# Kernel tuning notes

Measured on AMD Instinct MI355X. Metric: run time of the kernel, lower is better.

## Reference

```python
import math
import jax, jax.numpy as jnp
import numpy as np

N_HEADS = 16
D_EMBED = 1024
D_HEAD = D_EMBED // N_HEADS
BATCH = 2
SEQ = 2048


def setup_inputs() -> dict:
    key = jax.random.key(0)
    k1, k2, k3 = jax.random.split(key, 3)
    scale = 1.0 / math.sqrt(D_EMBED)
    return {
        "x": jax.random.normal(k1, (1, BATCH, SEQ, D_EMBED), dtype=jnp.float32),
        "w_in": jax.random.normal(k2, (3 * D_EMBED, D_EMBED), dtype=jnp.float32) * scale,
        "b_in": jnp.zeros((3 * D_EMBED,), dtype=jnp.float32),
        "w_out": jax.random.normal(k3, (D_EMBED, D_EMBED), dtype=jnp.float32) * scale,
        "b_out": jnp.zeros((D_EMBED,), dtype=jnp.float32),
        "causal_mask": 1,
    }


def reference(x, w_in, b_in, w_out, b_out, causal_mask):
    lead, B, S, D = x.shape  # lead == 1
    H, dh = N_HEADS, D_HEAD
    # fused QKV projection (torch Linear: x @ W^T + b)
    qkv = jnp.einsum("lbsd,ed->lbse", x, w_in) + b_in
    q, k, v = jnp.split(qkv, 3, axis=-1)
    # [1,B,S,D] -> [B,H,S,dh]
    def to_heads(t):
        return t.reshape(B, S, H, dh).transpose(0, 2, 1, 3)
    q, k, v = to_heads(q), to_heads(k), to_heads(v)
    # scaled dot-product attention with optional causal mask
    scores = jnp.einsum("bhqd,bhkd->bhqk", q, k)
    if causal_mask:
        mask = jnp.triu(jnp.ones((S, S), dtype=bool), k=1)
        scores = jnp.where(mask, -jnp.inf, scores)
    scores = scores / math.sqrt(dh)
    attn = jax.nn.softmax(scores, axis=-1)
    out = jnp.einsum("bhqk,bhkd->bhqd", attn, v)
    out = out.transpose(0, 2, 1, 3).reshape(lead, B, S, D)
    return jnp.einsum("lbsd,ed->lbse", out, w_out) + b_out
```

## Files before the change

kernel.cpp:

```cpp
#include <hip/hip_runtime.h>
#include <hip/hip_bf16.h>
#include <stdint.h>

#define S_LEN 2048
#define D_EMB 1024
#define NHEAD 16
#define DHEAD 64
#define NBATCH 2
#define MROWS 4096

typedef __attribute__((ext_vector_type(8))) short bf16x8;
typedef __attribute__((ext_vector_type(4))) float f32x4;
typedef unsigned short u16;
typedef unsigned int u32;

__device__ __forceinline__ u16 f2bf(float f) {
  union { float f; u32 u; } v; v.f = f;
  u32 r = v.u + 0x7fffu + ((v.u >> 16) & 1u);
  return (u16)(r >> 16);
}

__device__ __forceinline__ void gl_lds16(const void* g, void* l) {
  __builtin_amdgcn_global_load_lds(
      (const __attribute__((address_space(1))) u32*)g,
      (__attribute__((address_space(3))) u32*)l, 16, 0, 0);
}

__device__ __forceinline__ int swz(int o) { return o ^ (((o >> 7) & 7) << 4); }

__global__ void cast_f32_bf16(const float* __restrict__ in, u16* __restrict__ out, int n4) {
  int i = blockIdx.x * blockDim.x + threadIdx.x;
  if (i < n4) {
    float4 v = reinterpret_cast<const float4*>(in)[i];
    ushort4 o;
    o.x = f2bf(v.x); o.y = f2bf(v.y); o.z = f2bf(v.z); o.w = f2bf(v.w);
    reinterpret_cast<ushort4*>(out)[i] = o;
  }
}

template <int EPI>
__launch_bounds__(512, 2)
__global__ void gemm_pipe(const u16* __restrict__ A, const u16* __restrict__ Bm,
                          const float* __restrict__ bias, int N,
                          u16* __restrict__ q_out, u16* __restrict__ k_out,
                          u16* __restrict__ vt_out, float* __restrict__ f_out) {
  __shared__ __align__(16) u16 As[4][128 * 64];
  __shared__ __align__(16) u16 Bs[4][128 * 64];
  const int K = 1024, NT = 16;
  const int t = threadIdx.x, w = t >> 6, lane = t & 63;
  const int lr = lane & 15, lg = lane >> 4;
  const int m0 = blockIdx.y * 128, n0 = blockIdx.x * 128;
  const int wr = w >> 2, wc = w & 3;

  f32x4 acc[4][2] = {};

  const int srow = w * 8 + (lane >> 3);
  const int scol = ((lane & 7) ^ (lane >> 3)) * 8;
  const u16* Asrc = A + (size_t)(m0 + srow) * K + scol;
  const u16* Bsrc = Bm + (size_t)(n0 + srow) * K + scol;

#define STAGEP(T)                                                        \
  do {                                                                   \
    const int _kt = (T) * 64, _bf = (T) & 3;                             \
    gl_lds16(Asrc + _kt, &As[_bf][w * 512]);                             \
    gl_lds16(Asrc + (size_t)64 * K + _kt, &As[_bf][4096 + w * 512]);     \
    gl_lds16(Bsrc + _kt, &Bs[_bf][w * 512]);                             \
    gl_lds16(Bsrc + (size_t)64 * K + _kt, &Bs[_bf][4096 + w * 512]);     \
  } while (0)

  const int xorv = (lane & 7) << 4;
  const int ofk[2] = {(lg * 16) ^ xorv, (64 + lg * 16) ^ xorv};

  STAGEP(0);
  STAGEP(1);
  STAGEP(2);

  for (int kt = 0; kt < NT; kt++) {
    if (kt < NT - 2)      asm volatile("s_waitcnt vmcnt(8)" ::: "memory");
    else if (kt == NT - 2) asm volatile("s_waitcnt vmcnt(4)" ::: "memory");
    else                   asm volatile("s_waitcnt vmcnt(0)" ::: "memory");
    __builtin_amdgcn_s_barrier();

    if (kt + 3 < NT) STAGEP(kt + 3);

    const char* Ab = (const char*)&As[kt & 3][0];
    const char* Bb = (const char*)&Bs[kt & 3][0];
#pragma unroll
    for (int ks = 0; ks < 2; ks++) {
      bf16x8 bfr[2];
#pragma unroll
      for (int j = 0; j < 2; j++)
        bfr[j] = *(const bf16x8*)(Bb + (wc * 32 + j * 16 + lr) * 128 + ofk[ks]);
#pragma unroll
      for (int i = 0; i < 4; i++) {
        bf16x8 af = *(const bf16x8*)(Ab + (wr * 64 + i * 16 + lr) * 128 + ofk[ks]);
#pragma unroll
        for (int j = 0; j < 2; j++)
          acc[i][j] = __builtin_amdgcn_mfma_f32_16x16x32_bf16(af, bfr[j], acc[i][j], 0, 0, 0);
      }
    }
  }
#undef STAGEP

#pragma unroll
  for (int j = 0; j < 2; j++) {
    const int n = n0 + wc * 32 + j * 16 + lr;
    const float bv = bias[n];
    const int which = n >> 10, nn = n & 1023;
    const int h = nn >> 6, d = nn & 63;
#pragma unroll
    for (int i = 0; i < 4; i++) {
#pragma unroll
      for (int r = 0; r < 4; r++) {
        const int m = m0 + wr * 64 + i * 16 + lg * 4 + r;
        float v = acc[i][j][r] + bv;
        if (EPI == 0) {
          const int b = m >> 11, s = m & 2047;
          if (which == 0)
            q_out[(size_t)(((b * NHEAD + h) * S_LEN) + s) * DHEAD + d] = f2bf(v * 0.180336880f);
          else if (which == 1)
            k_out[(size_t)(((b * NHEAD + h) * S_LEN) + s) * DHEAD + d] = f2bf(v);
          else
            vt_out[(size_t)(((b * NHEAD + h) * DHEAD) + d) * S_LEN + s] = f2bf(v);
        } else {
          f_out[(size_t)m * N + n] = v;
        }
      }
    }
  }
}

__launch_bounds__(512, 2)
__global__ void attn_kernel(const u16* __restrict__ Qg, const u16* __restrict__ Kg,
                            const u16* __restrict__ Vtg, u16* __restrict__ AO,
                            const int* __restrict__ causal) {
  __shared__ __align__(16) u16 Kt[2][64 * 64];
  __shared__ __align__(16) u16 Vt[2][64 * 64];
  __shared__ __align__(16) u16 Pl[8][16 * 72];

  const int t = threadIdx.x, w = t >> 6, lane = t & 63;
  const int lr = lane & 15, lg = lane >> 4;
  const int nqt = (int)gridDim.x;
  const int qt = ((int)blockIdx.y < 16) ? (nqt - 1 - (int)blockIdx.x) : (int)blockIdx.x;
  const int bh = blockIdx.y;
  const size_t bh_off = (size_t)bh * S_LEN * DHEAD;
  const int cz = *causal;
  const int q0 = qt * 128;
  const int nk = cz ? (2 * qt + 2) : (S_LEN / 64);

  bf16x8 ones;
#pragma unroll
  for (int e = 0; e < 8; e++) ones[e] = (short)16256;

  {
    const char* qb = (const char*)(Qg + bh_off + (size_t)q0 * DHEAD);
#pragma unroll
    for (int c = 0; c < 2; c++) {
      int drel = c * 8192 + w * 1024 + lane * 16;
      gl_lds16(qb + swz(drel), (char*)&Kt[0][0] + c * 8192 + w * 1024);
    }
  }
  __syncthreads();
  bf16x8 qf[2];
#pragma unroll
  for (int ks = 0; ks < 2; ks++) {
    int rq = w * 16 + lr;
    qf[ks] = *(const bf16x8*)((const char*)&Kt[0][0] + swz(rq * 128 + ks * 64 + lg * 16));
  }
  __syncthreads();

  auto stageK = [&](int kt, int buf) {
    const char* kb = (const char*)(Kg + bh_off + (size_t)kt * 64 * DHEAD);
    int drel = w * 1024 + lane * 16;
    gl_lds16(kb + swz(drel), (char*)&Kt[buf][0] + w * 1024);
  };
  auto stageV = [&](int kt, int buf) {
    int drel = w * 1024 + lane * 16;
    int o = swz(drel);
    int row = o >> 7, colb = o & 127;
    const char* vb = (const char*)Vtg +
                     (((size_t)bh * DHEAD + row) * S_LEN + (size_t)kt * 64) * 2 + colb;
    gl_lds16(vb, (char*)&Vt[buf][0] + w * 1024);
  };

  float m_run[4], l_run[4];
  f32x4 o_acc[4] = {};
#pragma unroll
  for (int r = 0; r < 4; r++) { m_run[r] = -INFINITY; l_run[r] = 0.f; }

  stageK(0, 0);
  stageV(0, 0);
  __syncthreads();
  int cur = 0;

  for (int kt = 0; kt < nk; kt++) {
    if (kt + 1 < nk) {
      stageK(kt + 1, cur ^ 1);
      stageV(kt + 1, cur ^ 1);
    }

    f32x4 s[4] = {};
#pragma unroll
    for (int nf = 0; nf < 4; nf++) {
#pragma unroll
      for (int ks = 0; ks < 2; ks++) {
        int r = nf * 16 + lr;
        bf16x8 kf = *(const bf16x8*)((const char*)&Kt[cur][0] + swz(r * 128 + ks * 64 + lg * 16));
        s[nf] = __builtin_amdgcn_mfma_f32_16x16x32_bf16(qf[ks], kf, s[nf], 0, 0, 0);
      }
    }

    if (cz && (kt * 64 + 63 > q0 + w * 16)) {
#pragma unroll
      for (int nf = 0; nf < 4; nf++)
#pragma unroll
        for (int r = 0; r < 4; r++) {
          int kv = kt * 64 + nf * 16 + lr;
          int qr = q0 + w * 16 + lg * 4 + r;
          if (kv > qr) s[nf][r] = -INFINITY;
        }
    }

    float lmax[4];
#pragma unroll
    for (int r = 0; r < 4; r++)
      lmax[r] = fmaxf(fmaxf(s[0][r], s[1][r]), fmaxf(s[2][r], s[3][r]));
    float need = fmaxf(fmaxf(lmax[0] - m_run[0], lmax[1] - m_run[1]),
                       fmaxf(lmax[2] - m_run[2], lmax[3] - m_run[3]));
    if (!__all(need <= 8.0f)) {
      float rmax[4];
#pragma unroll
      for (int r = 0; r < 4; r++) rmax[r] = lmax[r];
#pragma unroll
      for (int mlt = 1; mlt < 16; mlt <<= 1)
#pragma unroll
        for (int r = 0; r < 4; r++) rmax[r] = fmaxf(rmax[r], __shfl_xor(rmax[r], mlt, 64));
#pragma unroll
      for (int r = 0; r < 4; r++) {
        float mn = fmaxf(m_run[r], rmax[r]);
        float scl = exp2f(m_run[r] - mn);
        m_run[r] = mn;
        l_run[r] *= scl;
#pragma unroll
        for (int nf = 0; nf < 4; nf++) o_acc[nf][r] *= scl;
      }
    }

#pragma unroll
    for (int nf = 0; nf < 4; nf++)
#pragma unroll
      for (int r = 0; r < 4; r++) {
        float p = exp2f(s[nf][r] - m_run[r]);
        Pl[w][(lg * 4 + r) * 72 + nf * 16 + lr] = f2bf(p);
      }

    asm volatile("s_waitcnt lgkmcnt(0)" ::: "memory");
    __builtin_amdgcn_sched_barrier(0);

    bf16x8 pf[2];
#pragma unroll
    for (int ks = 0; ks < 2; ks++)
      pf[ks] = *(const bf16x8*)&Pl[w][lr * 72 + ks * 32 + lg * 8];

    f32x4 lsum = {};
    lsum = __builtin_amdgcn_mfma_f32_16x16x32_bf16(pf[0], ones, lsum, 0, 0, 0);
    lsum = __builtin_amdgcn_mfma_f32_16x16x32_bf16(pf[1], ones, lsum, 0, 0, 0);

#pragma unroll
    for (int nf = 0; nf < 4; nf++) {
#pragma unroll
      for (int ks = 0; ks < 2; ks++) {
        int r = nf * 16 + lr;
        bf16x8 vf = *(const bf16x8*)((const char*)&Vt[cur][0] + swz(r * 128 + ks * 64 + lg * 16));
        o_acc[nf] = __builtin_amdgcn_mfma_f32_16x16x32_bf16(pf[ks], vf, o_acc[nf], 0, 0, 0);
      }
    }
#pragma unroll
    for (int r = 0; r < 4; r++) l_run[r] += lsum[r];

    __syncthreads();
    cur ^= 1;
  }

  const int b = bh >> 4, h = bh & 15;
#pragma unroll
  for (int nf = 0; nf < 4; nf++)
#pragma unroll
    for (int r = 0; r < 4; r++) {
      float v = o_acc[nf][r] / l_run[r];
      int qrow = q0 + w * 16 + lg * 4 + r;
      int d = nf * 16 + lr;
      AO[(size_t)(b * S_LEN + qrow) * D_EMB + h * DHEAD + d] = f2bf(v);
    }
}

extern "C" void kernel_launch(void* const* d_in, const int* in_sizes, int n_in,
                              void* d_out, int out_size, void* d_ws, size_t ws_size,
                              hipStream_t stream) {
  const float* x = (const float*)d_in[0];
  const float* w_in = (const float*)d_in[1];
  const float* b_in = (const float*)d_in[2];
  const float* w_out = (const float*)d_in[3];
  const float* b_out = (const float*)d_in[4];
  const int* causal = (const int*)d_in[5];
  float* out = (float*)d_out;

  char* p = (char*)d_ws;
  u16* xb = (u16*)p;  p += (size_t)MROWS * D_EMB * 2;
  u16* wib = (u16*)p; p += (size_t)3 * D_EMB * D_EMB * 2;
  u16* wob = (u16*)p; p += (size_t)D_EMB * D_EMB * 2;
  u16* Qg = (u16*)p;  p += (size_t)MROWS * D_EMB * 2;
  u16* Kg = (u16*)p;  p += (size_t)MROWS * D_EMB * 2;
  u16* Vtg = (u16*)p; p += (size_t)MROWS * D_EMB * 2;
  u16* AO = (u16*)p;  p += (size_t)MROWS * D_EMB * 2;

  {
    int n4 = MROWS * D_EMB / 4;
    cast_f32_bf16<<<(n4 + 255) / 256, 256, 0, stream>>>(x, xb, n4);
  }
  {
    int n4 = 3 * D_EMB * D_EMB / 4;
    cast_f32_bf16<<<(n4 + 255) / 256, 256, 0, stream>>>(w_in, wib, n4);
  }
  {
    int n4 = D_EMB * D_EMB / 4;
    cast_f32_bf16<<<(n4 + 255) / 256, 256, 0, stream>>>(w_out, wob, n4);
  }

  gemm_pipe<0><<<dim3(3 * D_EMB / 128, MROWS / 128), 512, 0, stream>>>(
      xb, wib, b_in, 3 * D_EMB, Qg, Kg, Vtg, nullptr);

  attn_kernel<<<dim3(S_LEN / 128, NBATCH * NHEAD), 512, 0, stream>>>(Qg, Kg, Vtg, AO, causal);

  gemm_pipe<1><<<dim3(D_EMB / 128, MROWS / 128), 512, 0, stream>>>(
      AO, wob, b_out, D_EMB, nullptr, nullptr, nullptr, out);
}
```

Before: 225.9 us.

## Replace QKV GEMM with 256x256-tile ping-pong kernel and XCD-aware block swizzle

Swaps the 128x128 4-stage QKV projection GEMM for a new 256x256-tile kernel. Each wave computes a 128x64 sub-tile in four phases, interleaving LDS fragment reads, the next tile's global-to-LDS loads, and MFMA bursts raised with s_setprio. Block IDs are remapped so consecutive blocks spread across XCDs to improve L2 reuse. The larger tiles cut global and LDS traffic per FLOP, but the grid shrinks to 192 blocks on a 256-CU device and the kernel adds many barriers and more register pressure.

```diff
diff --git a/kernel.cpp b/kernel.cpp
--- a/kernel.cpp
+++ b/kernel.cpp
@@ -27,6 +27,8 @@
 }
 
 __device__ __forceinline__ int swz(int o) { return o ^ (((o >> 7) & 7) << 4); }
+
+#define MFMA16(a, b, c) __builtin_amdgcn_mfma_f32_16x16x32_bf16((a), (b), (c), 0, 0, 0)
 
 __global__ void cast_f32_bf16(const float* __restrict__ in, u16* __restrict__ out, int n4) {
   int i = blockIdx.x * blockDim.x + threadIdx.x;
@@ -38,12 +40,160 @@
   }
 }
 
-template <int EPI>
 __launch_bounds__(512, 2)
-__global__ void gemm_pipe(const u16* __restrict__ A, const u16* __restrict__ Bm,
-                          const float* __restrict__ bias, int N,
-                          u16* __restrict__ q_out, u16* __restrict__ k_out,
-                          u16* __restrict__ vt_out, float* __restrict__ f_out) {
+__global__ void gemm8p_qkv(const u16* __restrict__ A, const u16* __restrict__ Bm,
+                           const float* __restrict__ bias,
+                           u16* __restrict__ q_out, u16* __restrict__ k_out,
+                           u16* __restrict__ vt_out) {
+  __shared__ __align__(16) u16 As[2][2][8192];
+  __shared__ __align__(16) u16 Bs[2][2][8192];
+  const int K = 1024;
+  const int t = threadIdx.x, w = t >> 6, lane = t & 63;
+  const int lr = lane & 15, lg = lane >> 4;
+
+  const int bid = (int)blockIdx.y * 12 + (int)blockIdx.x;
+  const int sbid = (bid & 7) * 24 + (bid >> 3);
+  const int bx = sbid % 12, by = sbid / 12;
+  const int m0 = by * 256, n0 = bx * 256;
+  const int wr = w >> 2, wc = w & 3;
+
+  f32x4 acc[8][4] = {};
+
+  const u16* Ab = A + (size_t)(m0 + w * 8 + (lane >> 3)) * K + ((lane & 7) ^ (lane >> 3)) * 8;
+  const u16* Bb = Bm + (size_t)(n0 + w * 8 + (lane >> 3)) * K + ((lane & 7) ^ (lane >> 3)) * 8;
+#define STG_A(TT, H, CC) \
+  gl_lds16(Ab + (size_t)((H)*128 + (CC)*64) * K + (TT)*64, &As[(TT)&1][H][(CC)*4096 + w * 512])
+#define STG_B(TT, H, CC) \
+  gl_lds16(Bb + (size_t)((H)*128 + (CC)*64) * K + (TT)*64, &Bs[(TT)&1][H][(CC)*4096 + w * 512])
+
+  const int xorv = (lane & 7) << 4;
+  const int ofk0 = (lg * 16) ^ xorv, ofk1 = (64 + lg * 16) ^ xorv;
+
+  STG_A(0, 0, 0); STG_A(0, 0, 1); STG_A(0, 1, 0); STG_A(0, 1, 1);
+  STG_B(0, 0, 0); STG_B(0, 0, 1); STG_B(0, 1, 0); STG_B(0, 1, 1);
+  asm volatile("s_waitcnt vmcnt(0)" ::: "memory");
+  __builtin_amdgcn_s_barrier();
+
+  bf16x8 aF[4][2];
+  bf16x8 bF[2][2][2];
+
+  for (int tt = 0; tt < 16; tt++) {
+    const char* Ah = (const char*)&As[tt & 1][wr][0];
+    const char* Bh = (const char*)&Bs[tt & 1][wc >> 1][0];
+    const int brow0 = (wc & 1) * 64;
+    const bool pf = (tt + 1) < 16;
+
+#pragma unroll
+    for (int i = 0; i < 4; i++) {
+      const int r = i * 16 + lr;
+      aF[i][0] = *(const bf16x8*)(Ah + r * 128 + ofk0);
+      aF[i][1] = *(const bf16x8*)(Ah + r * 128 + ofk1);
+    }
+#pragma unroll
+    for (int j = 0; j < 2; j++) {
+      const int r = brow0 + j * 16 + lr;
+      bF[0][j][0] = *(const bf16x8*)(Bh + r * 128 + ofk0);
+      bF[0][j][1] = *(const bf16x8*)(Bh + r * 128 + ofk1);
+    }
+    if (pf) { STG_A(tt + 1, 0, 0); STG_A(tt + 1, 0, 1); STG_A(tt + 1, 1, 0); STG_A(tt + 1, 1, 1); }
+    __builtin_amdgcn_s_barrier();
+    asm volatile("s_waitcnt lgkmcnt(0)" ::: "memory");
+    __builtin_amdgcn_sched_barrier(0);
+    __builtin_amdgcn_s_setprio(1);
+#pragma unroll
+    for (int i = 0; i < 4; i++)
+#pragma unroll
+      for (int j = 0; j < 2; j++) {
+        acc[i][j] = MFMA16(aF[i][0], bF[0][j][0], acc[i][j]);
+        acc[i][j] = MFMA16(aF[i][1], bF[0][j][1], acc[i][j]);
+      }
+    __builtin_amdgcn_s_setprio(0);
+    __builtin_amdgcn_s_barrier();
+
+#pragma unroll
+    for (int j = 0; j < 2; j++) {
+      const int r = brow0 + (2 + j) * 16 + lr;
+      bF[1][j][0] = *(const bf16x8*)(Bh + r * 128 + ofk0);
+      bF[1][j][1] = *(const bf16x8*)(Bh + r * 128 + ofk1);
+    }
+    if (pf) { STG_B(tt + 1, 0, 0); STG_B(tt + 1, 0, 1); STG_B(tt + 1, 1, 0); STG_B(tt + 1, 1, 1); }
+    __builtin_amdgcn_s_barrier();
+    asm volatile("s_waitcnt lgkmcnt(0)" ::: "memory");
+    __builtin_amdgcn_sched_barrier(0);
+    __builtin_amdgcn_s_setprio(1);
+#pragma unroll
+    for (int i = 0; i < 4; i++)
+#pragma unroll
+      for (int j = 0; j < 2; j++) {
+        acc[i][2 + j] = MFMA16(aF[i][0], bF[1][j][0], acc[i][2 + j]);
+        acc[i][2 + j] = MFMA16(aF[i][1], bF[1][j][1], acc[i][2 + j]);
+      }
+    __builtin_amdgcn_s_setprio(0);
+    __builtin_amdgcn_s_barrier();
+
+#pragma unroll
+    for (int i = 0; i < 4; i++) {
+      const int r = 64 + i * 16 + lr;
+      aF[i][0] = *(const bf16x8*)(Ah + r * 128 + ofk0);
+      aF[i][1] = *(const bf16x8*)(Ah + r * 128 + ofk1);
+    }
+    __builtin_amdgcn_s_barrier();
+    asm volatile("s_waitcnt lgkmcnt(0)" ::: "memory");
+    __builtin_amdgcn_sched_barrier(0);
+    __builtin_amdgcn_s_setprio(1);
+#pragma unroll
+    for (int i = 0; i < 4; i++)
+#pragma unroll
+      for (int j = 0; j < 2; j++) {
+        acc[4 + i][2 + j] = MFMA16(aF[i][0], bF[1][j][0], acc[4 + i][2 + j]);
+        acc[4 + i][2 + j] = MFMA16(aF[i][1], bF[1][j][1], acc[4 + i][2 + j]);
+      }
+    __builtin_amdgcn_s_setprio(0);
+    __builtin_amdgcn_s_barrier();
+
+    __builtin_amdgcn_s_setprio(1);
+#pragma unroll
+    for (int i = 0; i < 4; i++)
+#pragma unroll
+      for (int j = 0; j < 2; j++) {
+        acc[4 + i][j] = MFMA16(aF[i][0], bF[0][j][0], acc[4 + i][j]);
+        acc[4 + i][j] = MFMA16(aF[i][1], bF[0][j][1], acc[4 + i][j]);
+      }
+    __builtin_amdgcn_s_setprio(0);
+    asm volatile("s_waitcnt vmcnt(0)" ::: "memory");
+    __builtin_amdgcn_s_barrier();
+  }
+#undef STG_A
+#undef STG_B
+
+#pragma unroll
+  for (int j = 0; j < 4; j++) {
+    const int n = n0 + wc * 64 + j * 16 + lr;
+    const float bv = bias[n];
+    const int which = n >> 10, nn = n & 1023;
+    const int h = nn >> 6, d = nn & 63;
+#pragma unroll
+    for (int i = 0; i < 8; i++) {
+#pragma unroll
+      for (int r = 0; r < 4; r++) {
+        const int m = m0 + wr * 128 + i * 16 + lg * 4 + r;
+        const int b = m >> 11, s = m & 2047;
+        float v = acc[i][j][r] + bv;
+        if (which == 0)
+          q_out[(size_t)(((b * NHEAD + h) * S_LEN) + s) * DHEAD + d] = f2bf(v * 0.180336880f);
+        else if (which == 1)
+          k_out[(size_t)(((b * NHEAD + h) * S_LEN) + s) * DHEAD + d] = f2bf(v);
+        else
+          vt_out[(size_t)(((b * NHEAD + h) * DHEAD) + d) * S_LEN + s] = f2bf(v);
+      }
+    }
+  }
+}
+
+__launch_bounds__(512, 2)
+__global__ void gemm_pipe_f32(const u16* __restrict__ A, const u16* __restrict__ Bm,
+                              const float* __restrict__ bias, int N,
+                              float* __restrict__ f_out) {
   __shared__ __align__(16) u16 As[4][128 * 64];
   __shared__ __align__(16) u16 Bs[4][128 * 64];
   const int K = 1024, NT = 16;
@@ -76,7 +226,7 @@
   STAGEP(2);
 
   for (int kt = 0; kt < NT; kt++) {
-    if (kt < NT - 2)      asm volatile("s_waitcnt vmcnt(8)" ::: "memory");
+    if (kt < NT - 2)       asm volatile("s_waitcnt vmcnt(8)" ::: "memory");
     else if (kt == NT - 2) asm volatile("s_waitcnt vmcnt(4)" ::: "memory");
     else                   asm volatile("s_waitcnt vmcnt(0)" ::: "memory");
     __builtin_amdgcn_s_barrier();
@@ -96,7 +246,7 @@
         bf16x8 af = *(const bf16x8*)(Ab + (wr * 64 + i * 16 + lr) * 128 + ofk[ks]);
 #pragma unroll
         for (int j = 0; j < 2; j++)
-          acc[i][j] = __builtin_amdgcn_mfma_f32_16x16x32_bf16(af, bfr[j], acc[i][j], 0, 0, 0);
+          acc[i][j] = MFMA16(af, bfr[j], acc[i][j]);
       }
     }
   }
@@ -106,25 +256,12 @@
   for (int j = 0; j < 2; j++) {
     const int n = n0 + wc * 32 + j * 16 + lr;
     const float bv = bias[n];
-    const int which = n >> 10, nn = n & 1023;
-    const int h = nn >> 6, d = nn & 63;
 #pragma unroll
     for (int i = 0; i < 4; i++) {
 #pragma unroll
       for (int r = 0; r < 4; r++) {
         const int m = m0 + wr * 64 + i * 16 + lg * 4 + r;
-        float v = acc[i][j][r] + bv;
-        if (EPI == 0) {
-          const int b = m >> 11, s = m & 2047;
-          if (which == 0)
-            q_out[(size_t)(((b * NHEAD + h) * S_LEN) + s) * DHEAD + d] = f2bf(v * 0.180336880f);
-          else if (which == 1)
-            k_out[(size_t)(((b * NHEAD + h) * S_LEN) + s) * DHEAD + d] = f2bf(v);
-          else
-            vt_out[(size_t)(((b * NHEAD + h) * DHEAD) + d) * S_LEN + s] = f2bf(v);
-        } else {
-          f_out[(size_t)m * N + n] = v;
-        }
+        f_out[(size_t)m * N + n] = acc[i][j][r] + bv;
       }
     }
   }
@@ -206,7 +343,7 @@
       for (int ks = 0; ks < 2; ks++) {
         int r = nf * 16 + lr;
         bf16x8 kf = *(const bf16x8*)((const char*)&Kt[cur][0] + swz(r * 128 + ks * 64 + lg * 16));
-        s[nf] = __builtin_amdgcn_mfma_f32_16x16x32_bf16(qf[ks], kf, s[nf], 0, 0, 0);
+        s[nf] = MFMA16(qf[ks], kf, s[nf]);
       }
     }
 
@@ -263,8 +400,8 @@
       pf[ks] = *(const bf16x8*)&Pl[w][lr * 72 + ks * 32 + lg * 8];
 
     f32x4 lsum = {};
-    lsum = __builtin_amdgcn_mfma_f32_16x16x32_bf16(pf[0], ones, lsum, 0, 0, 0);
-    lsum = __builtin_amdgcn_mfma_f32_16x16x32_bf16(pf[1], ones, lsum, 0, 0, 0);
+    lsum = MFMA16(pf[0], ones, lsum);
+    lsum = MFMA16(pf[1], ones, lsum);
 
 #pragma unroll
     for (int nf = 0; nf < 4; nf++) {
@@ -272,7 +409,7 @@
       for (int ks = 0; ks < 2; ks++) {
         int r = nf * 16 + lr;
         bf16x8 vf = *(const bf16x8*)((const char*)&Vt[cur][0] + swz(r * 128 + ks * 64 + lg * 16));
-        o_acc[nf] = __builtin_amdgcn_mfma_f32_16x16x32_bf16(pf[ks], vf, o_acc[nf], 0, 0, 0);
+        o_acc[nf] = MFMA16(pf[ks], vf, o_acc[nf]);
       }
     }
 #pragma unroll
@@ -327,11 +464,11 @@
     cast_f32_bf16<<<(n4 + 255) / 256, 256, 0, stream>>>(w_out, wob, n4);
   }
 
-  gemm_pipe<0><<<dim3(3 * D_EMB / 128, MROWS / 128), 512, 0, stream>>>(
-      xb, wib, b_in, 3 * D_EMB, Qg, Kg, Vtg, nullptr);
+  gemm8p_qkv<<<dim3(3 * D_EMB / 256, MROWS / 256), 512, 0, stream>>>(
+      xb, wib, b_in, Qg, Kg, Vtg);
 
   attn_kernel<<<dim3(S_LEN / 128, NBATCH * NHEAD), 512, 0, stream>>>(Qg, Kg, Vtg, AO, causal);
 
-  gemm_pipe<1><<<dim3(D_EMB / 128, MROWS / 128), 512, 0, stream>>>(
-      AO, wob, b_out, D_EMB, nullptr, nullptr, nullptr, out);
-}
+  gemm_pipe_f32<<<dim3(D_EMB / 128, MROWS / 128), 512, 0, stream>>>(
+      AO, wob, b_out, D_EMB, out);
+}
```

Result: faster. 219.5 us (-2.8%).
